# Kernel optimization log

Hardware: AMD Instinct MI355X
Metric: run time of the kernel (lower is better)

## Reference

```python
import jax, jax.numpy as jnp
import numpy as np

EMB = 768
HEADS = 12
DH = EMB // HEADS


def setup_inputs() -> dict:
    key = jax.random.key(0)
    k = jax.random.split(key, 5)
    s = 0.02
    return {
        "x": jax.random.normal(k[0], (4, 2048, EMB), dtype=jnp.float32),
        "qkv_w": jax.random.normal(k[1], (3 * EMB, EMB), dtype=jnp.float32) * s,  # torch Linear weight [out,in]
        "qkv_b": jax.random.normal(k[2], (3 * EMB,), dtype=jnp.float32) * s,
        "proj_w": jax.random.normal(k[3], (EMB, EMB), dtype=jnp.float32) * s,
        "proj_b": jax.random.normal(k[4], (EMB,), dtype=jnp.float32) * s,
    }


def reference(x, qkv_w, qkv_b, proj_w, proj_b):
    b, n, _ = x.shape
    qkv = x @ qkv_w.T + qkv_b  # [b, n, 3*EMB]
    # rearrange 'b n (h d qkv) -> qkv b h n d'
    qkv = qkv.reshape(b, n, HEADS, DH, 3)
    qkv = jnp.transpose(qkv, (4, 0, 2, 1, 3))  # [3, b, h, n, d]
    q, k, v = qkv[0], qkv[1], qkv[2]
    e = jnp.einsum("bhqd,bhkd->bhqk", q, k)
    scale = jnp.float32(EMB) ** 0.5
    # NOTE: original divides by sqrt(emb_size) AFTER softmax (faithful to source)
    attn = jax.nn.softmax(e, axis=-1) / scale
    out = jnp.einsum("bhqk,bhkd->bhqd", attn, v)
    out = jnp.transpose(out, (0, 2, 1, 3)).reshape(b, n, EMB)  # 'b h n d -> b n (h d)'
    return out @ proj_w.T + proj_b
```

## Files before the change

### kernel.cpp

```cpp
#include <hip/hip_runtime.h>
#include <hip/hip_bf16.h>

typedef unsigned short ushort_t;
typedef __attribute__((ext_vector_type(8))) short s16x8;
typedef __attribute__((ext_vector_type(4))) float f32x4;
typedef __attribute__((ext_vector_type(16))) float f32x16;
typedef __attribute__((ext_vector_type(4))) unsigned int u32x4;

#define EMB 768
#define HEADS 12
#define DH 64
#define BATCH 4
#define SEQ 2048
#define MTOK (BATCH*SEQ)
#define NQKV (3*EMB)
#define NBH (BATCH*HEADS)
#define LOG2E 1.44269504088896f

#define N4X (MTOK*EMB/4)
#define N4W (NQKV*EMB/4)
#define N4P (EMB*EMB/4)

__device__ __forceinline__ ushort_t f2bf(float f) {
  unsigned u = __float_as_uint(f);
  u += 0x7fffu + ((u >> 16) & 1u);
  return (ushort_t)(u >> 16);
}
__device__ __forceinline__ unsigned pk2bf(float a, float b) {
  return (unsigned)f2bf(a) | ((unsigned)f2bf(b) << 16);
}
__device__ __forceinline__ unsigned cvtpk(float lo, float hi_) {
  unsigned d;
  asm("v_cvt_pk_bf16_f32 %0, %1, %2" : "=v"(d) : "v"(lo), "v"(hi_));
  return d;
}

__device__ __forceinline__ void gload_lds16(const void* g, void* l) {
  __builtin_amdgcn_global_load_lds(
      (const __attribute__((address_space(1))) unsigned*)g,
      (__attribute__((address_space(3))) unsigned*)l, 16, 0, 0);
}

__global__ void cvt_all(const float* __restrict__ x, const float* __restrict__ qkv_w,
                        const float* __restrict__ qkv_b, const float* __restrict__ proj_w,
                        ushort_t* __restrict__ xb, ushort_t* __restrict__ wqkv,
                        float* __restrict__ bias_p, ushort_t* __restrict__ wproj) {
  const int i = blockIdx.x * blockDim.x + threadIdx.x;
  if (i < N4X) {
    const float4 v = reinterpret_cast<const float4*>(x)[i];
    reinterpret_cast<uint2*>(xb)[i] = make_uint2(pk2bf(v.x, v.y), pk2bf(v.z, v.w));
  } else if (i < N4X + N4W) {
    const int j = i - N4X;
    const int srcrow = j / 192;
    const int c4 = j - srcrow * 192;
    const int h = srcrow / 192;
    const int rem = srcrow - h * 192;
    const int d = rem / 3;
    const int which = rem - d * 3;
    const int dstrow = which * 768 + h * 64 + d;
    const float4 v = reinterpret_cast<const float4*>(qkv_w)[j];
    reinterpret_cast<uint2*>(wqkv)[dstrow * 192 + c4] =
        make_uint2(pk2bf(v.x, v.y), pk2bf(v.z, v.w));
    if (c4 == 0) bias_p[dstrow] = qkv_b[srcrow];
  } else {
    const int j = i - N4X - N4W;
    const float4 v = reinterpret_cast<const float4*>(proj_w)[j];
    reinterpret_cast<uint2*>(wproj)[j] = make_uint2(pk2bf(v.x, v.y), pk2bf(v.z, v.w));
  }
}

#define TM 128
#define TN 128
#define BKG 64
#define GSTEPS 12

template<int MODE>
__global__ __launch_bounds__(256, 2) void gemm_bt(
    const ushort_t* __restrict__ A, const ushort_t* __restrict__ BT,
    const float* __restrict__ bias, float* __restrict__ Cf,
    ushort_t* __restrict__ Qd, ushort_t* __restrict__ Kd, ushort_t* __restrict__ Vt,
    int M, int N, int K)
{
  __shared__ alignas(16) ushort_t As[2][TM*BKG];
  __shared__ alignas(16) ushort_t Bs[2][TN*BKG];
  const int t = threadIdx.x;
  const int w = t >> 6, l = t & 63, g = l >> 4, r = l & 15;
  const int wr = w >> 1, wc = w & 1;
  int lin = blockIdx.y * gridDim.x + blockIdx.x;
  const int cpx = (gridDim.x * gridDim.y) >> 3;
  lin = (lin & 7) * cpx + (lin >> 3);
  const int m0 = (lin / gridDim.x) * TM, n0 = (lin - (lin / gridDim.x) * gridDim.x) * TN;

  f32x4 acc[4][4] = {};

#define GSTAGE(bufc, st)                                                           \
  {                                                                                \
    const int kt = (st) * BKG;                                                     \
    _Pragma("unroll")                                                              \
    for (int p = 0; p < 4; ++p) {                                                  \
      const int off = (t + p*256) * 16;                     \
      const int row = off >> 7;                                  \
      const int scb = (off & 127) ^ ((row & 7) << 4);                              \
      gload_lds16(A  + (size_t)(m0+row)*K + kt + (scb>>1), (char*)&As[bufc][0] + off); \
      gload_lds16(BT + (size_t)(n0+row)*K + kt + (scb>>1), (char*)&Bs[bufc][0] + off); \
    }                                                                              \
  }

#define GCOMP(bufc)                                                                \
  {                                                                                \
    s16x8 fa[4][2], fb[4][2];                                                      \
    _Pragma("unroll")                                                              \
    for (int mi = 0; mi < 4; ++mi)                                                 \
      _Pragma("unroll")                                                            \
      for (int kk = 0; kk < 2; ++kk) {                                             \
        const int ra = wr*64 + mi*16 + r;                                          \
        fa[mi][kk] = *(const s16x8*)((const char*)&As[bufc][0] + ra*128 +          \
                                     ((g*16 + kk*64) ^ ((ra&7)<<4)));              \
        const int rb = wc*64 + mi*16 + r;                                          \
        fb[mi][kk] = *(const s16x8*)((const char*)&Bs[bufc][0] + rb*128 +          \
                                     ((g*16 + kk*64) ^ ((rb&7)<<4)));              \
      }                                                                            \
    __builtin_amdgcn_s_setprio(1);                                                 \
    _Pragma("unroll")                                                              \
    for (int mi = 0; mi < 4; ++mi)                                                 \
      _Pragma("unroll")                                                            \
      for (int ni = 0; ni < 4; ++ni) {                                             \
        acc[mi][ni] = __builtin_amdgcn_mfma_f32_16x16x32_bf16(                     \
            fa[mi][0], fb[ni][0], acc[mi][ni], 0, 0, 0);                           \
        acc[mi][ni] = __builtin_amdgcn_mfma_f32_16x16x32_bf16(                     \
            fa[mi][1], fb[ni][1], acc[mi][ni], 0, 0, 0);                           \
      }                                                                            \
    __builtin_amdgcn_s_setprio(0);                                                 \
  }

#define GITER(cur, st)                                                             \
  {                                                                                \
    asm volatile("s_barrier" ::: "memory");                                        \
    { const int s1 = (st) + 1 < GSTEPS ? (st) + 1 : GSTEPS - 1;                    \
      GSTAGE((cur) ^ 1, s1); }                                                     \
    asm volatile("s_waitcnt vmcnt(8)" ::: "memory");                               \
    asm volatile("s_barrier" ::: "memory");                                        \
    GCOMP(cur);                                                                    \
  }

  GSTAGE(0, 0);
#pragma unroll
  for (int s = 0; s < GSTEPS; ++s) GITER(s & 1, s);
#undef GITER
#undef GCOMP
#undef GSTAGE

#pragma unroll
  for (int ni = 0; ni < 4; ++ni) {
    const int col = n0 + wc*64 + ni*16 + r;
    const float bv = bias[col];
    if (MODE == 0) {
#pragma unroll
      for (int mi = 0; mi < 4; ++mi)
#pragma unroll
        for (int q = 0; q < 4; ++q) {
          const int rowg = m0 + wr*64 + mi*16 + g*4 + q;
          Cf[(size_t)rowg * N + col] = acc[mi][ni][q] + bv;
        }
    } else {
      const int which = col / 768;
      const int h_ = (col - which * 768) >> 6;
      const int d_ = col & 63;
      if (which == 2) {
#pragma unroll
        for (int mi = 0; mi < 4; ++mi) {
          const int nn0 = m0 + wr*64 + mi*16 + g*4;
          const int bb = nn0 >> 11, nl = nn0 & 2047;
          const int np0 = (nl & ~12) | ((nl & 4) << 1) | ((nl & 8) >> 1);
          uint2 u;
          u.x = pk2bf(acc[mi][ni][0] + bv, acc[mi][ni][1] + bv);
          u.y = pk2bf(acc[mi][ni][2] + bv, acc[mi][ni][3] + bv);
          *reinterpret_cast<uint2*>(Vt + ((size_t)(bb*HEADS + h_)*DH + d_)*SEQ + np0) = u;
        }
      } else {
        ushort_t* dst = (which == 0) ? Qd : Kd;
        const float sc = (which == 0) ? LOG2E : 1.0f;
#pragma unroll
        for (int mi = 0; mi < 4; ++mi)
#pragma unroll
          for (int q = 0; q < 4; ++q) {
            const int rowg = m0 + wr*64 + mi*16 + g*4 + q;
            const int bb = rowg >> 11, nn = rowg & 2047;
            dst[((size_t)(bb*HEADS + h_)*SEQ + nn)*DH + d_] =
                f2bf((acc[mi][ni][q] + bv) * sc);
          }
      }
    }
  }
}

#define NTIL 32

__global__ __launch_bounds__(256, 3) void attn_fwd(
    const ushort_t* __restrict__ Qd, const ushort_t* __restrict__ Kd,
    const ushort_t* __restrict__ Vt, ushort_t* __restrict__ Oa)
{
  __shared__ alignas(16) char L[3][16384];
  char* Lc = &L[0][0];

  const int t = threadIdx.x;
  const int w = t >> 6, l = t & 63;
  const int c31 = l & 31, hi = l >> 5;
  const int blk = blockIdx.x;
  const int logical = (blk & 7) * 96 + (blk >> 3);
  const int bh = logical >> 4;
  const int qt = logical & 15;
  const int q0 = qt * 128 + w * 32;
  const int b = bh / HEADS, h = bh - b * HEADS;

  const ushort_t* Qp = Qd + (size_t)bh * SEQ * DH;
  const ushort_t* Kp = Kd + (size_t)bh * SEQ * DH;
  const ushort_t* Vp = Vt + (size_t)bh * DH * SEQ;

  s16x8 qf[4];
  {
    const ushort_t* qp = Qp + (size_t)(q0 + c31) * DH + hi * 8;
#pragma unroll
    for (int c = 0; c < 4; ++c) qf[c] = *(const s16x8*)(qp + c * 16);
  }

  f32x16 oacc0 = {}, oacc1 = {};
  float ps0 = 0.f, ps1 = 0.f, ps2 = 0.f, ps3 = 0.f;

  const int ldsb = hi * 1024 + c31 * 16;
  const ushort_t* ksrc0 = Kp + (size_t)l * DH + w * 16;
  const ushort_t* vsrc0 = Vp + (size_t)l * SEQ + w * 16;
  char* kdst0 = Lc + w * 2048 + l * 16;

#define STAGE(bufc, tile_)                                                         \
  {                                                                                \
    const int tl = (tile_);                                                        \
    const ushort_t* ks = ksrc0 + (size_t)tl * (64 * DH);                           \
    const ushort_t* vs = vsrc0 + tl * 64;                                          \
    char* kd = kdst0 + (bufc) * 16384;                                             \
    gload_lds16(ks,     kd);                                                       \
    gload_lds16(ks + 8, kd + 1024);                                                \
    gload_lds16(vs,     kd + 8192);                                                \
    gload_lds16(vs + 8, kd + 9216);                                                \
  }

#define KGROUP(bufc, kg)                                                           \
  {                                                                                \
    const char* base = Lc + (bufc) * 16384 + ldsb;                                 \
    s16x8 kf0 = *(const s16x8*)(base + ((kg)*512 + 0*2048));                       \
    s16x8 kf1 = *(const s16x8*)(base + ((kg)*512 + 1*2048));                       \
    s16x8 kf2 = *(const s16x8*)(base + ((kg)*512 + 2*2048));                       \
    s16x8 kf3 = *(const s16x8*)(base + ((kg)*512 + 3*2048));                       \
    s16x8 va00 = *(const s16x8*)(base + (8192 + (kg)*4096 + 0*2048 + 0*512));      \
    s16x8 va01 = *(const s16x8*)(base + (8192 + (kg)*4096 + 1*2048 + 0*512));      \
    s16x8 va10 = *(const s16x8*)(base + (8192 + (kg)*4096 + 0*2048 + 1*512));      \
    s16x8 va11 = *(const s16x8*)(base + (8192 + (kg)*4096 + 1*2048 + 1*512));      \
    __builtin_amdgcn_s_setprio(1);                                                 \
    f32x16 s = {};                                                                 \
    s = __builtin_amdgcn_mfma_f32_32x32x16_bf16(kf0, qf[0], s, 0, 0, 0);           \
    s = __builtin_amdgcn_mfma_f32_32x32x16_bf16(kf1, qf[1], s, 0, 0, 0);           \
    s = __builtin_amdgcn_mfma_f32_32x32x16_bf16(kf2, qf[2], s, 0, 0, 0);           \
    s = __builtin_amdgcn_mfma_f32_32x32x16_bf16(kf3, qf[3], s, 0, 0, 0);           \
    __builtin_amdgcn_s_setprio(0);                                                 \
    float pe[16];                                                                  \
    _Pragma("unroll")                                                              \
    for (int r2 = 0; r2 < 16; ++r2) pe[r2] = __builtin_amdgcn_exp2f(s[r2]);        \
    ps0 += (pe[0]  + pe[1])  + (pe[2]  + pe[3]);                                   \
    ps1 += (pe[4]  + pe[5])  + (pe[6]  + pe[7]);                                   \
    ps2 += (pe[8]  + pe[9])  + (pe[10] + pe[11]);                                  \
    ps3 += (pe[12] + pe[13]) + (pe[14] + pe[15]);                                  \
    u32x4 f0u = { cvtpk(pe[0],  pe[1]),  cvtpk(pe[2],  pe[3]),                     \
                  cvtpk(pe[4],  pe[5]),  cvtpk(pe[6],  pe[7]) };                   \
    u32x4 f1u = { cvtpk(pe[8],  pe[9]),  cvtpk(pe[10], pe[11]),                    \
                  cvtpk(pe[12], pe[13]), cvtpk(pe[14], pe[15]) };                  \
    const s16x8 pf0 = __builtin_bit_cast(s16x8, f0u);                              \
    const s16x8 pf1 = __builtin_bit_cast(s16x8, f1u);                              \
    __builtin_amdgcn_s_setprio(1);                                                 \
    oacc0 = __builtin_amdgcn_mfma_f32_32x32x16_bf16(va00, pf0, oacc0, 0, 0, 0);    \
    oacc0 = __builtin_amdgcn_mfma_f32_32x32x16_bf16(va01, pf1, oacc0, 0, 0, 0);    \
    oacc1 = __builtin_amdgcn_mfma_f32_32x32x16_bf16(va10, pf0, oacc1, 0, 0, 0);    \
    oacc1 = __builtin_amdgcn_mfma_f32_32x32x16_bf16(va11, pf1, oacc1, 0, 0, 0);    \
    __builtin_amdgcn_s_setprio(0);                                                 \
  }

#define ITER(bufcur, bufn2, tt)                                                    \
  {                                                                                \
    asm volatile("s_barrier" ::: "memory");                                        \
    const int nt2 = (tt) + 2 < NTIL ? (tt) + 2 : NTIL - 1;                         \
    STAGE(bufn2, nt2);                                                             \
    asm volatile("s_waitcnt vmcnt(8)" ::: "memory");                               \
    asm volatile("s_barrier" ::: "memory");                                        \
    KGROUP(bufcur, 0);                                                             \
    KGROUP(bufcur, 1);                                                             \
  }

  STAGE(0, 0);
  STAGE(1, 1);
  for (int tt = 0; tt < NTIL - 2; tt += 3) {
    ITER(0, 2, tt);
    ITER(1, 0, tt + 1);
    ITER(2, 1, tt + 2);
  }
  ITER(0, 2, 30);
  ITER(1, 0, 31);
#undef ITER
#undef KGROUP
#undef STAGE

  const float psum = (ps0 + ps1) + (ps2 + ps3);
  const float lt = psum + __shfl_xor(psum, 32);
  const float scale = 0.036084391824351615f / lt;

  ushort_t* op = Oa + ((size_t)(b * SEQ + q0 + c31)) * EMB + h * DH;
#pragma unroll
  for (int f = 0; f < 2; ++f) {
    const f32x16& o = f ? oacc1 : oacc0;
#pragma unroll
    for (int rq = 0; rq < 4; ++rq) {
      const int dbase = f * 32 + 8 * rq + 4 * hi;
      uint2 u;
      u.x = pk2bf(o[rq*4+0] * scale, o[rq*4+1] * scale);
      u.y = pk2bf(o[rq*4+2] * scale, o[rq*4+3] * scale);
      *reinterpret_cast<uint2*>(op + dbase) = u;
    }
  }
}

extern "C" void kernel_launch(void* const* d_in, const int* in_sizes, int n_in,
                              void* d_out, int out_size, void* d_ws, size_t ws_size,
                              hipStream_t stream) {
  const float* x      = (const float*)d_in[0];
  const float* qkv_w  = (const float*)d_in[1];
  const float* qkv_b  = (const float*)d_in[2];
  const float* proj_w = (const float*)d_in[3];
  const float* proj_b = (const float*)d_in[4];
  float* out = (float*)d_out;

  ushort_t* xb    = (ushort_t*)d_ws;
  ushort_t* wqkv  = xb    + (size_t)MTOK*EMB;
  ushort_t* wproj = wqkv  + (size_t)NQKV*EMB;
  ushort_t* Qd    = wproj + (size_t)EMB*EMB;
  ushort_t* Kd    = Qd    + (size_t)MTOK*EMB;
  ushort_t* Vt    = Kd    + (size_t)MTOK*EMB;
  ushort_t* Oa    = Vt    + (size_t)MTOK*EMB;
  float*    biasp = (float*)(Oa + (size_t)MTOK*EMB);

  cvt_all<<<(N4X + N4W + N4P) / 256, 256, 0, stream>>>(
      x, qkv_w, qkv_b, proj_w, xb, wqkv, biasp, wproj);

  gemm_bt<1><<<dim3(NQKV/TN, MTOK/TM), 256, 0, stream>>>(
      xb, wqkv, biasp, nullptr, Qd, Kd, Vt, MTOK, NQKV, EMB);

  attn_fwd<<<768, 256, 0, stream>>>(Qd, Kd, Vt, Oa);

  gemm_bt<0><<<dim3(EMB/TN, MTOK/TM), 256, 0, stream>>>(
      Oa, wproj, proj_b, out, nullptr, nullptr, nullptr, MTOK, EMB, EMB);
}
```

Before: 141.9 us.

## Load V fragments directly from global into registers instead of staging through LDS

The attention kernel no longer stages V tiles through shared memory. Each wave now loads its V MFMA operands straight from global memory into registers at the start of every iteration. Only K stays in the triple-buffered LDS ring, which halves LDS use and removes the V LDS reads. The cost is that all four waves of a block fetch the same V data from global memory or L2, and each load is issued just before it is used, so its latency may be exposed. The waitcnt threshold is raised to account for the extra in-flight loads.

```diff
diff --git a/kernel.cpp b/kernel.cpp
--- a/kernel.cpp
+++ b/kernel.cpp
@@ -200,7 +200,7 @@
     const ushort_t* __restrict__ Qd, const ushort_t* __restrict__ Kd,
     const ushort_t* __restrict__ Vt, ushort_t* __restrict__ Oa)
 {
-  __shared__ alignas(16) char L[3][16384];
+  __shared__ alignas(16) char L[3][8192];
   char* Lc = &L[0][0];
 
   const int t = threadIdx.x;
@@ -229,32 +229,25 @@
 
   const int ldsb = hi * 1024 + c31 * 16;
   const ushort_t* ksrc0 = Kp + (size_t)l * DH + w * 16;
-  const ushort_t* vsrc0 = Vp + (size_t)l * SEQ + w * 16;
+  const ushort_t* vsrc0 = Vp + (size_t)c31 * SEQ + hi * 8;
+  const ushort_t* vsrc1 = vsrc0 + (size_t)32 * SEQ;
   char* kdst0 = Lc + w * 2048 + l * 16;
 
 #define STAGE(bufc, tile_)                                                         \
   {                                                                                \
-    const int tl = (tile_);                                                        \
-    const ushort_t* ks = ksrc0 + (size_t)tl * (64 * DH);                           \
-    const ushort_t* vs = vsrc0 + tl * 64;                                          \
-    char* kd = kdst0 + (bufc) * 16384;                                             \
+    const ushort_t* ks = ksrc0 + (size_t)(tile_) * (64 * DH);                      \
+    char* kd = kdst0 + (bufc) * 8192;                                              \
     gload_lds16(ks,     kd);                                                       \
     gload_lds16(ks + 8, kd + 1024);                                                \
-    gload_lds16(vs,     kd + 8192);                                                \
-    gload_lds16(vs + 8, kd + 9216);                                                \
-  }
-
-#define KGROUP(bufc, kg)                                                           \
-  {                                                                                \
-    const char* base = Lc + (bufc) * 16384 + ldsb;                                 \
+  }
+
+#define KGROUP(bufc, kg, VA)                                                       \
+  {                                                                                \
+    const char* base = Lc + (bufc) * 8192 + ldsb;                                  \
     s16x8 kf0 = *(const s16x8*)(base + ((kg)*512 + 0*2048));                       \
     s16x8 kf1 = *(const s16x8*)(base + ((kg)*512 + 1*2048));                       \
     s16x8 kf2 = *(const s16x8*)(base + ((kg)*512 + 2*2048));                       \
     s16x8 kf3 = *(const s16x8*)(base + ((kg)*512 + 3*2048));                       \
-    s16x8 va00 = *(const s16x8*)(base + (8192 + (kg)*4096 + 0*2048 + 0*512));      \
-    s16x8 va01 = *(const s16x8*)(base + (8192 + (kg)*4096 + 1*2048 + 0*512));      \
-    s16x8 va10 = *(const s16x8*)(base + (8192 + (kg)*4096 + 0*2048 + 1*512));      \
-    s16x8 va11 = *(const s16x8*)(base + (8192 + (kg)*4096 + 1*2048 + 1*512));      \
     __builtin_amdgcn_s_setprio(1);                                                 \
     f32x16 s = {};                                                                 \
     s = __builtin_amdgcn_mfma_f32_32x32x16_bf16(kf0, qf[0], s, 0, 0, 0);           \
@@ -276,22 +269,31 @@
     const s16x8 pf0 = __builtin_bit_cast(s16x8, f0u);                              \
     const s16x8 pf1 = __builtin_bit_cast(s16x8, f1u);                              \
     __builtin_amdgcn_s_setprio(1);                                                 \
-    oacc0 = __builtin_amdgcn_mfma_f32_32x32x16_bf16(va00, pf0, oacc0, 0, 0, 0);    \
-    oacc0 = __builtin_amdgcn_mfma_f32_32x32x16_bf16(va01, pf1, oacc0, 0, 0, 0);    \
-    oacc1 = __builtin_amdgcn_mfma_f32_32x32x16_bf16(va10, pf0, oacc1, 0, 0, 0);    \
-    oacc1 = __builtin_amdgcn_mfma_f32_32x32x16_bf16(va11, pf1, oacc1, 0, 0, 0);    \
+    oacc0 = __builtin_amdgcn_mfma_f32_32x32x16_bf16(VA[0], pf0, oacc0, 0, 0, 0);   \
+    oacc0 = __builtin_amdgcn_mfma_f32_32x32x16_bf16(VA[1], pf1, oacc0, 0, 0, 0);   \
+    oacc1 = __builtin_amdgcn_mfma_f32_32x32x16_bf16(VA[2], pf0, oacc1, 0, 0, 0);   \
+    oacc1 = __builtin_amdgcn_mfma_f32_32x32x16_bf16(VA[3], pf1, oacc1, 0, 0, 0);   \
     __builtin_amdgcn_s_setprio(0);                                                 \
   }
 
 #define ITER(bufcur, bufn2, tt)                                                    \
   {                                                                                \
+    s16x8 va0[4], va1[4];                                                          \
+    {                                                                              \
+      const ushort_t* v0 = vsrc0 + (tt) * 64;                                      \
+      const ushort_t* v1 = vsrc1 + (tt) * 64;                                      \
+      va0[0] = *(const s16x8*)(v0);        va0[1] = *(const s16x8*)(v0 + 16);      \
+      va0[2] = *(const s16x8*)(v1);        va0[3] = *(const s16x8*)(v1 + 16);      \
+      va1[0] = *(const s16x8*)(v0 + 32);   va1[1] = *(const s16x8*)(v0 + 48);      \
+      va1[2] = *(const s16x8*)(v1 + 32);   va1[3] = *(const s16x8*)(v1 + 48);      \
+    }                                                                              \
     asm volatile("s_barrier" ::: "memory");                                        \
-    const int nt2 = (tt) + 2 < NTIL ? (tt) + 2 : NTIL - 1;                         \
-    STAGE(bufn2, nt2);                                                             \
-    asm volatile("s_waitcnt vmcnt(8)" ::: "memory");                               \
+    { const int nt2 = (tt) + 2 < NTIL ? (tt) + 2 : NTIL - 1;                       \
+      STAGE(bufn2, nt2); }                                                         \
+    asm volatile("s_waitcnt vmcnt(12)" ::: "memory");                              \
     asm volatile("s_barrier" ::: "memory");                                        \
-    KGROUP(bufcur, 0);                                                             \
-    KGROUP(bufcur, 1);                                                             \
+    KGROUP(bufcur, 0, va0);                                                        \
+    KGROUP(bufcur, 1, va1);                                                        \
   }
 
   STAGE(0, 0);
```

After: 217.4 us. +53.2%, slower.
